# Optimization experiments

Measured on AMD Instinct MI355X. Metric: run time of the kernel, lower is better.

Reference implementation:

```python
import jax, jax.numpy as jnp
import numpy as np

NUM_CODES = 128
BETA = 0.25


def conv1d(x, w, b):
    # x: (B, C, T), w: (O, I, K) torch layout, 'same' padding for k=3
    y = jax.lax.conv_general_dilated(x, w, window_strides=(1,), padding=[(1, 1)],
                                     dimension_numbers=('NCH', 'OIH', 'NCH'))
    return y + b[None, :, None]


def setup_inputs() -> dict:
    key = jax.random.key(0)
    ks = jax.random.split(key, 8)
    B, C, T, K = 16, 192, 8192, NUM_CODES
    fan = 1.0 / np.sqrt(C * 3)
    inp = {
        'x': jax.random.normal(ks[0], (B, C, T), jnp.float32),
        'enc_w1': jax.random.normal(ks[1], (C, C, 3), jnp.float32) * fan,
        'enc_b1': jnp.zeros((C,), jnp.float32),
        'enc_w2': jax.random.normal(ks[2], (C, C, 3), jnp.float32) * fan,
        'enc_b2': jnp.zeros((C,), jnp.float32),
        'emb': jax.random.normal(ks[3], (K, C), jnp.float32) * (1.0 / K),
        'dec_w1': jax.random.normal(ks[4], (C, C, 3), jnp.float32) * fan,
        'dec_b1': jnp.zeros((C,), jnp.float32),
        'dec_w2': jax.random.normal(ks[5], (C, C, 3), jnp.float32) * fan,
        'dec_b2': jnp.zeros((C,), jnp.float32),
        'dec_w3': jax.random.normal(ks[6], (C, C, 3), jnp.float32) * fan,
        'dec_b3': jnp.zeros((C,), jnp.float32),
    }
    return inp


def vector_quantize(z_e, emb):
    # z_e: (B, C, T) -> tokens (B*T, C)
    B, C, T = z_e.shape
    z = jnp.transpose(z_e, (0, 2, 1)).reshape(-1, C)          # (N, C)
    # squared distances ||z||^2 + ||e||^2 - 2 z.e
    d = (jnp.sum(z * z, axis=1, keepdims=True)
         + jnp.sum(emb * emb, axis=1)[None, :]
         - 2.0 * (z @ emb.T))                                  # (N, K)
    idx = jnp.argmin(d, axis=1)                                # (N,)
    z_q = emb[idx]                                             # (N, C) gather
    # loss = ||sg(z_q) - z||^2*... standard: codebook + beta*commitment
    loss = (jnp.mean((jax.lax.stop_gradient(z_q) - z) ** 2)
            + BETA * jnp.mean((z_q - jax.lax.stop_gradient(z)) ** 2))
    # perplexity of code usage
    n = z.shape[0]
    counts = jnp.zeros((emb.shape[0],), z.dtype).at[idx].add(1.0)
    probs = counts / n
    perplexity = jnp.exp(-jnp.sum(probs * jnp.log(probs + 1e-10)))
    # straight-through
    z_q = z + jax.lax.stop_gradient(z_q - z)
    z_q = jnp.transpose(z_q.reshape(B, T, C), (0, 2, 1))
    return loss, z_q, perplexity, idx


def reference(x, enc_w1, enc_b1, enc_w2, enc_b2, emb,
              dec_w1, dec_b1, dec_w2, dec_b2, dec_w3, dec_b3):
    # encoder: conv -> relu -> conv
    z_e = conv1d(jax.nn.relu(conv1d(x, enc_w1, enc_b1)), enc_w2, enc_b2)
    embedding_loss, z_q, perplexity, _ = vector_quantize(z_e, emb)
    # NOTE: source forward decodes z_e (not z_q) — reproduced faithfully
    h = jax.nn.relu(conv1d(z_e, dec_w1, dec_b1))
    h = jax.nn.relu(conv1d(h, dec_w2, dec_b2))
    x_hat = conv1d(h, dec_w3, dec_b3)
    return embedding_loss, x_hat, perplexity
```

## Files before the change

### kernel.cpp

```cpp
#include <hip/hip_runtime.h>
#include <hip/hip_bf16.h>
#include <stdint.h>

typedef short s16x8 __attribute__((ext_vector_type(8)));
typedef float f32x4 __attribute__((ext_vector_type(4)));
typedef unsigned int u32;
typedef unsigned short u16;

#define CCH 192
#define APITCH 200
#define NCODES 128
#define HALO 9
#define RPB 8216
#define LEAD 12
#define TOK 256
#define AROWS 274
#define CHS 16384

__device__ __forceinline__ u16 f2b(float f) {
  u32 u = __builtin_bit_cast(u32, f);
  u = (u + 0x7fffu + ((u >> 16) & 1u)) >> 16;
  return (u16)u;
}
__device__ __forceinline__ float b2f(u16 h) {
  return __builtin_bit_cast(float, ((u32)h) << 16);
}
__device__ __forceinline__ void gld16(const void* g, void* l) {
  __builtin_amdgcn_global_load_lds(
      (const __attribute__((address_space(1))) void*)g,
      (__attribute__((address_space(3))) void*)l, 16, 0, 0);
}

__global__ __launch_bounds__(256) void k_tin(const float* __restrict__ x, u16* __restrict__ xtp,
                                             int B, int T) {
  __shared__ float tile[32][36];
  int nt = T >> 5;
  int bid = blockIdx.x;
  int b = bid / (6 * nt);
  int rem = bid % (6 * nt);
  int cb = rem / nt, tb = rem % nt;
  int tid = threadIdx.x;
  {
    int c = tid >> 3, seg = tid & 7;
    const float* src = x + ((size_t)b * CCH + cb * 32 + c) * T + tb * 32 + seg * 4;
    float4 v = *(const float4*)src;
    tile[c][seg * 4 + 0] = v.x; tile[c][seg * 4 + 1] = v.y;
    tile[c][seg * 4 + 2] = v.z; tile[c][seg * 4 + 3] = v.w;
  }
  __syncthreads();
  {
    int t = tid >> 3, cs = tid & 7;
    u16* dst = xtp + ((size_t)(b * RPB + LEAD + tb * 32 + t)) * APITCH + cb * 32 + cs * 4;
    ushort4 o;
    o.x = f2b(tile[cs * 4 + 0][t]); o.y = f2b(tile[cs * 4 + 1][t]);
    o.z = f2b(tile[cs * 4 + 2][t]); o.w = f2b(tile[cs * 4 + 3][t]);
    *(ushort4*)dst = o;
  }
}

__global__ __launch_bounds__(256) void k_padz(u16* __restrict__ xtp) {
  int b = blockIdx.x;
  for (int i = threadIdx.x; i < 24 * 25; i += 256) {
    int r = i / 25, c = i - (i / 25) * 25;
    int row = (r < 12) ? r : (RPB - 12 + (r - 12));
    uint4 z = {0u, 0u, 0u, 0u};
    *(uint4*)((char*)xtp + ((size_t)(b * RPB + row)) * 400 + c * 16) = z;
  }
}

__global__ __launch_bounds__(256) void k_wconv(const float* __restrict__ w, u16* __restrict__ dst) {
  int i = blockIdx.x * 256 + threadIdx.x;
  if (i >= 3 * CCH * CCH) return;
  int cb = i / 18432;
  int r = i - cb * 18432;
  int k = r / 6144;
  int r2 = r - k * 6144;
  int o = r2 / 32, il = r2 - o * 32;
  dst[(size_t)(cb * 3 + k) * (CHS / 2) + (il >> 3) * 1536 + o * 8 + (il & 7)] =
      f2b(w[(o * CCH + cb * 32 + il) * 3 + k]);
}

__global__ __launch_bounds__(64) void k_emb(const float* __restrict__ emb, u16* __restrict__ embp,
                                            float* __restrict__ e2) {
  int code = blockIdx.x, lane = threadIdx.x;
  float s = 0.f;
  for (int j = lane * 3; j < lane * 3 + 3; ++j) {
    float v = emb[code * CCH + j];
    int cb = j >> 5, il = j & 31;
    embp[(size_t)cb * 4096 + (il >> 3) * 1024 + code * 8 + (il & 7)] = f2b(v);
    s += v * v;
  }
  #pragma unroll
  for (int m = 1; m < 64; m <<= 1) s += __shfl_xor(s, m, 64);
  if (lane == 0) e2[code] = s;
}

__global__ void k_zero(int* hist, double* dsum) {
  int t = threadIdx.x;
  if (t < NCODES) hist[t] = 0;
  if (t == 0) *dsum = 0.0;
}

__device__ __forceinline__ void issueW(const char* src, u16* dstb, int wv, int lane) {
  const char* s0 = src + wv * 2048 + lane * 16;
  char* d0 = (char*)dstb + wv * 2048 + lane * 16;
  gld16(s0, d0);
  gld16(s0 + 1024, d0 + 1024);
}
__device__ __forceinline__ void issueE(const char* src, u16* dstb, int tid) {
  gld16(src + tid * 16, (char*)dstb + tid * 16);
}

template<int G0, int F, int NEXT>
__device__ __forceinline__ void conv_phase(const char* __restrict__ wtp, const char* __restrict__ embp,
                                           const u16* __restrict__ arow, u16 (*wb)[8192],
                                           int oB, int lr, int lg, int wv, int lane, int tid,
                                           f32x4 (&acc)[F][3]) {
  #pragma unroll 2
  for (int s = 0; s < 18; ++s) {
    asm volatile("s_waitcnt vmcnt(0)" ::: "memory");
    __builtin_amdgcn_sched_barrier(0);
    __builtin_amdgcn_s_barrier();
    if (s < 17) issueW(wtp + (size_t)(G0 + s + 1) * CHS, wb[(s + 1) & 1], wv, lane);
    else if (NEXT == 1) issueW(wtp + (size_t)(G0 + 18) * CHS, wb[0], wv, lane);
    else if (NEXT == 2) issueE(embp, wb[0], tid);
    const int cb = s / 3, k = s - 3 * (s / 3);
    const u16* wq = wb[s & 1] + lg * 1536 + (oB + lr) * 8;
    const u16* ab = arow + k * APITCH + cb * 32;
    s16x8 af[F];
    #pragma unroll
    for (int m = 0; m < F; ++m)
      af[m] = *(const s16x8*)(ab + 16 * m * APITCH);
    #pragma unroll
    for (int nf = 0; nf < 3; ++nf) {
      s16x8 wf = *(const s16x8*)(wq + nf * 128);
      #pragma unroll
      for (int m = 0; m < F; ++m)
        acc[m][nf] = __builtin_amdgcn_mfma_f32_16x16x32_bf16(af[m], wf, acc[m][nf], 0, 0, 0);
    }
  }
}

template<int F, bool RELU>
__device__ __forceinline__ void writeback(u16* __restrict__ act, const f32x4 (&acc)[F][3],
                                          const float* bv, int oB, int lr, int lg, int rbase,
                                          int t0, int T, bool edge) {
  __builtin_amdgcn_s_barrier();
  if (!edge) {
    #pragma unroll
    for (int m = 0; m < F; ++m)
      #pragma unroll
      for (int nf = 0; nf < 3; ++nf) {
        int o = oB + nf * 16 + lr;
        #pragma unroll
        for (int r = 0; r < 4; ++r) {
          int row = rbase + 16 * m + lg * 4 + r;
          float v = acc[m][nf][r] + bv[nf];
          if (RELU) v = fmaxf(v, 0.f);
          act[row * APITCH + o] = f2b(v);
        }
      }
  } else {
    #pragma unroll
    for (int m = 0; m < F; ++m)
      #pragma unroll
      for (int nf = 0; nf < 3; ++nf) {
        int o = oB + nf * 16 + lr;
        #pragma unroll
        for (int r = 0; r < 4; ++r) {
          int row = rbase + 16 * m + lg * 4 + r;
          int tok = t0 - HALO + row;
          float v = acc[m][nf][r] + bv[nf];
          if (RELU) v = fmaxf(v, 0.f);
          if (tok < 0 || tok >= T) v = 0.f;
          act[row * APITCH + o] = f2b(v);
        }
      }
  }
  asm volatile("s_waitcnt lgkmcnt(0)" ::: "memory");
  __builtin_amdgcn_s_barrier();
}

__global__ __launch_bounds__(512, 2) void k_fused(
    const char* __restrict__ xtp, const char* __restrict__ wtp,
    const float* __restrict__ eb1, const float* __restrict__ eb2,
    const float* __restrict__ db1, const float* __restrict__ db2, const float* __restrict__ db3,
    const char* __restrict__ embp, const float* __restrict__ e2,
    int* __restrict__ hist, double* __restrict__ dsum,
    float* __restrict__ xhat, int T) {
  __shared__ __align__(16) u16 act[AROWS * APITCH];
  __shared__ __align__(16) u16 wb[2][8192];
  __shared__ int hs[NCODES];
  __shared__ float wsum[8];
  const int tid = threadIdx.x;
  const int wv = tid >> 6, lane = tid & 63, lr = lane & 15, lg = lane >> 4;
  const int nw = wv & 3, mw = wv >> 2;
  const int bid = blockIdx.x;
  const int b = bid >> 5, tile = bid & 31;
  const int t0 = tile * TOK;
  const bool edge = (tile == 0) || (tile == 31);
  const int oB = nw * 48;
  const int rbase = 1 + mw * 128;
  const u16* arow = act + (rbase - 1 + lr) * APITCH + lg * 8;
  if (tid < NCODES) hs[tid] = 0;

  float bvv[5][3];
  #pragma unroll
  for (int nf = 0; nf < 3; ++nf) {
    int o = oB + nf * 16 + lr;
    bvv[0][nf] = eb1[o]; bvv[1][nf] = eb2[o];
    bvv[2][nf] = db1[o]; bvv[3][nf] = db2[o]; bvv[4][nf] = db3[o];
  }

  {
    const char* src = xtp + (size_t)(b * RPB + LEAD + t0 - HALO) * 400;
    #pragma unroll
    for (int s = 0; s < 14; ++s) {
      int c = tid + s * 512;
      if (c < AROWS * 25)
        gld16(src + (size_t)c * 16, (char*)act + (size_t)c * 16);
    }
  }
  issueW(wtp, wb[0], wv, lane);

  {
    f32x4 acc[9][3];
    #pragma unroll
    for (int m = 0; m < 9; ++m)
      #pragma unroll
      for (int n = 0; n < 3; ++n) acc[m][n] = f32x4{0.f, 0.f, 0.f, 0.f};
    conv_phase<0, 9, 1>(wtp, embp, arow, wb, oB, lr, lg, wv, lane, tid, acc);
    writeback<9, true>(act, acc, bvv[0], oB, lr, lg, rbase, t0, T, edge);
  }
  {
    f32x4 acc[9][3];
    #pragma unroll
    for (int m = 0; m < 9; ++m)
      #pragma unroll
      for (int n = 0; n < 3; ++n) acc[m][n] = f32x4{0.f, 0.f, 0.f, 0.f};
    conv_phase<18, 9, 2>(wtp, embp, arow, wb, oB, lr, lg, wv, lane, tid, acc);
    writeback<9, false>(act, acc, bvv[1], oB, lr, lg, rbase, t0, T, edge);
  }

  {
    f32x4 va0[8], va1[8];
    #pragma unroll
    for (int n = 0; n < 8; ++n) { va0[n] = f32x4{0.f,0.f,0.f,0.f}; va1[n] = f32x4{0.f,0.f,0.f,0.f}; }
    const int zr0 = 9 + wv * 32 + lr;
    #pragma unroll 2
    for (int s = 0; s < 6; ++s) {
      asm volatile("s_waitcnt vmcnt(0)" ::: "memory");
      __builtin_amdgcn_sched_barrier(0);
      __builtin_amdgcn_s_barrier();
      if (s < 5) issueE(embp + (s + 1) * 8192, wb[(s + 1) & 1], tid);
      else issueW(wtp + (size_t)36 * CHS, wb[0], wv, lane);
      const u16* eq = wb[s & 1] + lg * 1024 + lr * 8;
      s16x8 az0 = *(const s16x8*)(act + zr0 * APITCH + s * 32 + lg * 8);
      s16x8 az1 = *(const s16x8*)(act + (zr0 + 16) * APITCH + s * 32 + lg * 8);
      #pragma unroll
      for (int nf = 0; nf < 8; ++nf) {
        s16x8 ef = *(const s16x8*)(eq + nf * 128);
        va0[nf] = __builtin_amdgcn_mfma_f32_16x16x32_bf16(az0, ef, va0[nf], 0, 0, 0);
        va1[nf] = __builtin_amdgcn_mfma_f32_16x16x32_bf16(az1, ef, va1[nf], 0, 0, 0);
      }
    }
    float e2v[8];
    #pragma unroll
    for (int nf = 0; nf < 8; ++nf) e2v[nf] = e2[nf * 16 + lr];
    float dpart = 0.f;
    #pragma unroll
    for (int rg = 0; rg < 2; ++rg) {
      float z2 = 0.f;
      const u16* zr = act + (zr0 + rg * 16) * APITCH + lg * 48;
      #pragma unroll
      for (int j = 0; j < 48; j += 8) {
        s16x8 vv = *(const s16x8*)(zr + j);
        #pragma unroll
        for (int e = 0; e < 8; ++e) { float f = b2f((u16)vv[e]); z2 += f * f; }
      }
      z2 += __shfl_xor(z2, 16, 64);
      z2 += __shfl_xor(z2, 32, 64);
      float smin[4]; int imin[4];
      #pragma unroll
      for (int r = 0; r < 4; ++r) { smin[r] = 3.4e38f; imin[r] = 0; }
      #pragma unroll
      for (int nf = 0; nf < 8; ++nf) {
        int code = nf * 16 + lr;
        #pragma unroll
        for (int r = 0; r < 4; ++r) {
          float sc = e2v[nf] - 2.f * (rg ? va1[nf][r] : va0[nf][r]);
          if (sc < smin[r]) { smin[r] = sc; imin[r] = code; }
        }
      }
      #pragma unroll
      for (int m = 1; m < 16; m <<= 1) {
        #pragma unroll
        for (int r = 0; r < 4; ++r) {
          float so = __shfl_xor(smin[r], m, 64);
          int io = __shfl_xor(imin[r], m, 64);
          if (so < smin[r] || (so == smin[r] && io < imin[r])) { smin[r] = so; imin[r] = io; }
        }
      }
      #pragma unroll
      for (int r = 0; r < 4; ++r) {
        float z2t = __shfl(z2, lg * 4 + r, 64);
        if (lr == 0) {
          dpart += z2t + smin[r];
          atomicAdd(&hs[imin[r]], 1);
        }
      }
    }
    #pragma unroll
    for (int m = 1; m < 64; m <<= 1) dpart += __shfl_xor(dpart, m, 64);
    if (lane == 0) wsum[wv] = dpart;
    asm volatile("s_waitcnt lgkmcnt(0)" ::: "memory");
    __builtin_amdgcn_s_barrier();
    if (tid == 0) {
      double tot = 0.0;
      #pragma unroll
      for (int w = 0; w < 8; ++w) tot += (double)wsum[w];
      atomicAdd(dsum, tot);
    }
    if (tid < NCODES && hs[tid] > 0) atomicAdd(&hist[tid], hs[tid]);
  }

  {
    f32x4 acc[9][3];
    #pragma unroll
    for (int m = 0; m < 9; ++m)
      #pragma unroll
      for (int n = 0; n < 3; ++n) acc[m][n] = f32x4{0.f, 0.f, 0.f, 0.f};
    conv_phase<36, 9, 1>(wtp, embp, arow, wb, oB, lr, lg, wv, lane, tid, acc);
    writeback<9, true>(act, acc, bvv[2], oB, lr, lg, rbase, t0, T, edge);
  }
  {
    f32x4 acc[9][3];
    #pragma unroll
    for (int m = 0; m < 9; ++m)
      #pragma unroll
      for (int n = 0; n < 3; ++n) acc[m][n] = f32x4{0.f, 0.f, 0.f, 0.f};
    conv_phase<54, 9, 1>(wtp, embp, arow, wb, oB, lr, lg, wv, lane, tid, acc);
    writeback<9, true>(act, acc, bvv[3], oB, lr, lg, rbase, t0, T, edge);
  }

  f32x4 acc5[8][3];
  #pragma unroll
  for (int m = 0; m < 8; ++m)
    #pragma unroll
    for (int n = 0; n < 3; ++n) acc5[m][n] = f32x4{0.f, 0.f, 0.f, 0.f};
  {
    const u16* arow3 = act + (8 + mw * 128 + lr) * APITCH + lg * 8;
    conv_phase<72, 8, 0>(wtp, embp, arow3, wb, oB, lr, lg, wv, lane, tid, acc5);
  }

  float* ft = (float*)act;
  float* dstb = xhat + (size_t)b * CCH * T + t0;
  #pragma unroll
  for (int p = 0; p < 2; ++p) {
    __builtin_amdgcn_s_barrier();
    if ((nw >> 1) == p) {
      #pragma unroll
      for (int m = 0; m < 8; ++m)
        #pragma unroll
        for (int nf = 0; nf < 3; ++nf) {
          int o = (nw & 1) * 48 + nf * 16 + lr;
          #pragma unroll
          for (int r = 0; r < 4; ++r) {
            int tl = mw * 128 + 16 * m + lg * 4 + r;
            ft[o * 260 + tl] = acc5[m][nf][r] + bvv[4][nf];
          }
        }
    }
    asm volatile("s_waitcnt lgkmcnt(0)" ::: "memory");
    __builtin_amdgcn_s_barrier();
    #pragma unroll
    for (int i = 0; i < 48; ++i) {
      int s = tid + i * 512;
      int o = s >> 8, tl = s & 255;
      dstb[(size_t)(o + p * 96) * T + tl] = ft[o * 260 + tl];
    }
  }
}

__global__ __launch_bounds__(128) void k_fin(const int* __restrict__ hist,
                                             const double* __restrict__ dsum,
                                             float* __restrict__ out, int N, int ppos) {
  __shared__ float H[NCODES];
  int t = threadIdx.x;
  float p = (float)hist[t] / (float)N;
  H[t] = p * logf(p + 1e-10f);
  __syncthreads();
  if (t == 0) {
    float s = 0.f;
    for (int i = 0; i < NCODES; ++i) s += H[i];
    out[ppos] = expf(-s);
    out[0] = (float)(1.25 * (*dsum) / ((double)N * (double)CCH));
  }
}

extern "C" void kernel_launch(void* const* d_in, const int* in_sizes, int n_in,
                              void* d_out, int out_size, void* d_ws, size_t ws_size,
                              hipStream_t stream) {
  const int B = 16, T = 8192, N = B * T;
  const float* x   = (const float*)d_in[0];
  const float* ew1 = (const float*)d_in[1];
  const float* eb1 = (const float*)d_in[2];
  const float* ew2 = (const float*)d_in[3];
  const float* eb2 = (const float*)d_in[4];
  const float* emb = (const float*)d_in[5];
  const float* dw1 = (const float*)d_in[6];
  const float* db1 = (const float*)d_in[7];
  const float* dw2 = (const float*)d_in[8];
  const float* db2 = (const float*)d_in[9];
  const float* dw3 = (const float*)d_in[10];
  const float* db3 = (const float*)d_in[11];

  char* ws = (char*)d_ws;
  char*  xtp  = ws;
  char*  wtp  = ws + 52583424;
  char*  embp = ws + 54057984;
  float* e2   = (float*)(ws + 54107136);
  int*   hist = (int*)(ws + 54107648);
  double* dsum = (double*)(ws + 54108160);

  const int wblocks = (3 * CCH * CCH + 255) / 256;
  const int TCH = 18 * (CHS / 2);
  k_wconv<<<wblocks, 256, 0, stream>>>(ew1, (u16*)wtp);
  k_wconv<<<wblocks, 256, 0, stream>>>(ew2, (u16*)wtp + TCH);
  k_wconv<<<wblocks, 256, 0, stream>>>(dw1, (u16*)wtp + 2 * TCH);
  k_wconv<<<wblocks, 256, 0, stream>>>(dw2, (u16*)wtp + 3 * TCH);
  k_wconv<<<wblocks, 256, 0, stream>>>(dw3, (u16*)wtp + 4 * TCH);
  k_emb<<<NCODES, 64, 0, stream>>>(emb, (u16*)embp, e2);
  k_zero<<<1, 256, 0, stream>>>(hist, dsum);
  k_padz<<<B, 256, 0, stream>>>((u16*)xtp);
  k_tin<<<B * 6 * (T / 32), 256, 0, stream>>>(x, (u16*)xtp, B, T);

  k_fused<<<B * (T / TOK), 512, 0, stream>>>(xtp, wtp, eb1, eb2, db1, db2, db3,
                                             embp, e2, hist, dsum, (float*)d_out + 1, T);
  k_fin<<<1, 128, 0, stream>>>(hist, dsum, (float*)d_out, N, out_size - 1);
}
```

Baseline: 273.6 us.

## Fully unroll conv steps with inline-asm LDS reads and prefetch next activation fragments

The 18-step conv loop becomes a fully unrolled recursive template. Activation and weight LDS reads are issued through inline ds_read_b128 with immediate offsets, and the next step's activation fragments are prefetched into a double-buffered register array before the current step's MFMAs run. Explicit lgkmcnt waits let those reads overlap the MFMA chain. To fit the extra fragment registers, launch bounds drop to one 512-thread block per CU, which lowers occupancy and raises the risk of register pressure.

```diff
diff --git a/kernel.cpp b/kernel.cpp
--- a/kernel.cpp
+++ b/kernel.cpp
@@ -111,34 +111,56 @@
   gld16(src + tid * 16, (char*)dstb + tid * 16);
 }
 
+template<int F, int S, int M>
+__device__ __forceinline__ void af_load(u32 aaddr, s16x8 (&a)[2][F]) {
+  constexpr int cb = S / 3, k = S - 3 * (S / 3);
+  constexpr int imm = (16 * M + k) * 400 + cb * 64;
+  asm volatile("ds_read_b128 %0, %1 offset:%2" : "=v"(a[S & 1][M]) : "v"(aaddr), "i"(imm));
+  if constexpr (M + 1 < F) af_load<F, S, M + 1>(aaddr, a);
+}
+template<int NF>
+__device__ __forceinline__ void wf_load(u32 wq, s16x8 (&wf)[3]) {
+  asm volatile("ds_read_b128 %0, %1 offset:%2" : "=v"(wf[NF]) : "v"(wq), "i"(NF * 256));
+  if constexpr (NF + 1 < 3) wf_load<NF + 1>(wq, wf);
+}
+
+template<int G0, int F, int NEXT, int S>
+__device__ __forceinline__ void cstep(const char* __restrict__ wtp, const char* __restrict__ embp,
+                                      u16 (*wb)[8192], u32 aaddr, u32 wq0, u32 wq1,
+                                      int wv, int lane, int tid,
+                                      s16x8 (&a)[2][F], f32x4 (&acc)[F][3]) {
+  asm volatile("s_waitcnt vmcnt(0)" ::: "memory");
+  __builtin_amdgcn_sched_barrier(0);
+  __builtin_amdgcn_s_barrier();
+  if constexpr (S < 17) issueW(wtp + (size_t)(G0 + S + 1) * CHS, wb[(S + 1) & 1], wv, lane);
+  else if constexpr (NEXT == 1) issueW(wtp + (size_t)(G0 + 18) * CHS, wb[0], wv, lane);
+  else if constexpr (NEXT == 2) issueE(embp, wb[0], tid);
+  if constexpr (S == 0) af_load<F, 0, 0>(aaddr, a);
+  s16x8 wf[3];
+  wf_load<0>((S & 1) ? wq1 : wq0, wf);
+  if constexpr (S < 17) {
+    af_load<F, S + 1, 0>(aaddr, a);
+    if constexpr (F == 9) asm volatile("s_waitcnt lgkmcnt(9)" ::: "memory");
+    else                  asm volatile("s_waitcnt lgkmcnt(8)" ::: "memory");
+  } else {
+    asm volatile("s_waitcnt lgkmcnt(0)" ::: "memory");
+  }
+  __builtin_amdgcn_sched_barrier(0);
+  #pragma unroll
+  for (int nf = 0; nf < 3; ++nf)
+    #pragma unroll
+    for (int m = 0; m < F; ++m)
+      acc[m][nf] = __builtin_amdgcn_mfma_f32_16x16x32_bf16(a[S & 1][m], wf[nf], acc[m][nf], 0, 0, 0);
+  if constexpr (S + 1 < 18)
+    cstep<G0, F, NEXT, S + 1>(wtp, embp, wb, aaddr, wq0, wq1, wv, lane, tid, a, acc);
+}
+
 template<int G0, int F, int NEXT>
 __device__ __forceinline__ void conv_phase(const char* __restrict__ wtp, const char* __restrict__ embp,
-                                           const u16* __restrict__ arow, u16 (*wb)[8192],
-                                           int oB, int lr, int lg, int wv, int lane, int tid,
-                                           f32x4 (&acc)[F][3]) {
-  #pragma unroll 2
-  for (int s = 0; s < 18; ++s) {
-    asm volatile("s_waitcnt vmcnt(0)" ::: "memory");
-    __builtin_amdgcn_sched_barrier(0);
-    __builtin_amdgcn_s_barrier();
-    if (s < 17) issueW(wtp + (size_t)(G0 + s + 1) * CHS, wb[(s + 1) & 1], wv, lane);
-    else if (NEXT == 1) issueW(wtp + (size_t)(G0 + 18) * CHS, wb[0], wv, lane);
-    else if (NEXT == 2) issueE(embp, wb[0], tid);
-    const int cb = s / 3, k = s - 3 * (s / 3);
-    const u16* wq = wb[s & 1] + lg * 1536 + (oB + lr) * 8;
-    const u16* ab = arow + k * APITCH + cb * 32;
-    s16x8 af[F];
-    #pragma unroll
-    for (int m = 0; m < F; ++m)
-      af[m] = *(const s16x8*)(ab + 16 * m * APITCH);
-    #pragma unroll
-    for (int nf = 0; nf < 3; ++nf) {
-      s16x8 wf = *(const s16x8*)(wq + nf * 128);
-      #pragma unroll
-      for (int m = 0; m < F; ++m)
-        acc[m][nf] = __builtin_amdgcn_mfma_f32_16x16x32_bf16(af[m], wf, acc[m][nf], 0, 0, 0);
-    }
-  }
+                                           u16 (*wb)[8192], u32 aaddr, u32 wq0, u32 wq1,
+                                           int wv, int lane, int tid, f32x4 (&acc)[F][3]) {
+  s16x8 a[2][F];
+  cstep<G0, F, NEXT, 0>(wtp, embp, wb, aaddr, wq0, wq1, wv, lane, tid, a, acc);
 }
 
 template<int F, bool RELU>
@@ -181,7 +203,7 @@
   __builtin_amdgcn_s_barrier();
 }
 
-__global__ __launch_bounds__(512, 2) void k_fused(
+__global__ __launch_bounds__(512, 1) void k_fused(
     const char* __restrict__ xtp, const char* __restrict__ wtp,
     const float* __restrict__ eb1, const float* __restrict__ eb2,
     const float* __restrict__ db1, const float* __restrict__ db2, const float* __restrict__ db3,
@@ -201,8 +223,11 @@
   const bool edge = (tile == 0) || (tile == 31);
   const int oB = nw * 48;
   const int rbase = 1 + mw * 128;
-  const u16* arow = act + (rbase - 1 + lr) * APITCH + lg * 8;
   if (tid < NCODES) hs[tid] = 0;
+
+  const u32 aaddr = (u32)(uintptr_t)act + (u32)(((rbase - 1 + lr) * APITCH + lg * 8) * 2);
+  const u32 wq0 = (u32)(uintptr_t)wb[0] + (u32)((lg * 1536 + (oB + lr) * 8) * 2);
+  const u32 wq1 = wq0 + 16384u;
 
   float bvv[5][3];
   #pragma unroll
@@ -229,7 +254,7 @@
     for (int m = 0; m < 9; ++m)
       #pragma unroll
       for (int n = 0; n < 3; ++n) acc[m][n] = f32x4{0.f, 0.f, 0.f, 0.f};
-    conv_phase<0, 9, 1>(wtp, embp, arow, wb, oB, lr, lg, wv, lane, tid, acc);
+    conv_phase<0, 9, 1>(wtp, embp, wb, aaddr, wq0, wq1, wv, lane, tid, acc);
     writeback<9, true>(act, acc, bvv[0], oB, lr, lg, rbase, t0, T, edge);
   }
   {
@@ -238,7 +263,7 @@
     for (int m = 0; m < 9; ++m)
       #pragma unroll
       for (int n = 0; n < 3; ++n) acc[m][n] = f32x4{0.f, 0.f, 0.f, 0.f};
-    conv_phase<18, 9, 2>(wtp, embp, arow, wb, oB, lr, lg, wv, lane, tid, acc);
+    conv_phase<18, 9, 2>(wtp, embp, wb, aaddr, wq0, wq1, wv, lane, tid, acc);
     writeback<9, false>(act, acc, bvv[1], oB, lr, lg, rbase, t0, T, edge);
   }
 
@@ -330,7 +355,7 @@
     for (int m = 0; m < 9; ++m)
       #pragma unroll
       for (int n = 0; n < 3; ++n) acc[m][n] = f32x4{0.f, 0.f, 0.f, 0.f};
-    conv_phase<36, 9, 1>(wtp, embp, arow, wb, oB, lr, lg, wv, lane, tid, acc);
+    conv_phase<36, 9, 1>(wtp, embp, wb, aaddr, wq0, wq1, wv, lane, tid, acc);
     writeback<9, true>(act, acc, bvv[2], oB, lr, lg, rbase, t0, T, edge);
   }
   {
@@ -339,7 +364,7 @@
     for (int m = 0; m < 9; ++m)
       #pragma unroll
       for (int n = 0; n < 3; ++n) acc[m][n] = f32x4{0.f, 0.f, 0.f, 0.f};
-    conv_phase<54, 9, 1>(wtp, embp, arow, wb, oB, lr, lg, wv, lane, tid, acc);
+    conv_phase<54, 9, 1>(wtp, embp, wb, aaddr, wq0, wq1, wv, lane, tid, acc);
     writeback<9, true>(act, acc, bvv[3], oB, lr, lg, rbase, t0, T, edge);
   }
 
@@ -349,8 +374,8 @@
     #pragma unroll
     for (int n = 0; n < 3; ++n) acc5[m][n] = f32x4{0.f, 0.f, 0.f, 0.f};
   {
-    const u16* arow3 = act + (8 + mw * 128 + lr) * APITCH + lg * 8;
-    conv_phase<72, 8, 0>(wtp, embp, arow3, wb, oB, lr, lg, wv, lane, tid, acc5);
+    const u32 aaddr3 = (u32)(uintptr_t)act + (u32)(((8 + mw * 128 + lr) * APITCH + lg * 8) * 2);
+    conv_phase<72, 8, 0>(wtp, embp, wb, aaddr3, wq0, wq1, wv, lane, tid, acc5);
   }
 
   float* ft = (float*)act;
```

After: 235.3 us. 14.0% less time.
